# Kernel optimization log

Measured on AMD Instinct MI355X. Metric: run time of the kernel, lower is better.

Reference implementation:

```python
import jax, jax.numpy as jnp
import numpy as np

B, T, D, P, M = 4, 1024, 512, 64, 256


def setup_inputs() -> dict:
    key = jax.random.key(0)
    ks = jax.random.split(key, 10)
    s_d = 1.0 / np.sqrt(D)
    s_m = 1.0 / np.sqrt(M)
    s_p = 1.0 / np.sqrt(P)
    return {
        "inputs": jax.random.normal(ks[0], (B, T, D), dtype=jnp.float32),
        "ec": jax.random.normal(ks[1], (B, M), dtype=jnp.float32),
        "W1": jax.random.uniform(ks[2], (D, P), jnp.float32, -s_d, s_d),
        "b1": jax.random.uniform(ks[3], (P,), jnp.float32, -s_d, s_d),
        "W2": jax.random.uniform(ks[4], (D, P), jnp.float32, -s_d, s_d),
        "b2": jax.random.uniform(ks[5], (P,), jnp.float32, -s_d, s_d),
        "W3": jax.random.uniform(ks[6], (M, P), jnp.float32, -s_m, s_m),
        "b3": jax.random.uniform(ks[7], (P,), jnp.float32, -s_m, s_m),
        "wa_w": jax.random.uniform(ks[8], (P,), jnp.float32, -s_p, s_p),
        "wa_b": jax.random.uniform(ks[9], (), jnp.float32, -s_p, s_p),
    }


def reference(inputs, ec, W1, b1, W2, b2, W3, b3, wa_w, wa_b):
    # inputs: (B,T,D), ec: (B,M)
    w1h = inputs @ W1 + b1          # (B,T,P)
    w2h = inputs @ W2 + b2          # (B,T,P)
    w3e = ec @ W3 + b3              # (B,P)
    # Gt: (B,T,T,P) via broadcast add + tanh
    gt = jnp.tanh(w1h[:, :, None, :] + w2h[:, None, :, :] + w3e[:, None, None, :])
    at = jnp.einsum('btup,p->btu', gt, wa_w) + wa_b   # (B,T,T)
    at = jax.nn.softmax(at, axis=-1)
    out = jnp.einsum('btu,bud->btd', at, inputs)      # (B,T,D)
    return out
```

## Files before the change

### kernel.cpp

```cpp
#include <hip/hip_runtime.h>
#include <hip/hip_bf16.h>

constexpr int BB = 4;
constexpr int TT = 1024;
constexpr int DD = 512;
constexpr int PP = 64;
constexpr int MM = 256;

constexpr float CSCALE = 2.8853900817779268f;
constexpr float L2E = 1.4426950408889634f;

typedef __attribute__((ext_vector_type(8))) short v8s;
typedef __attribute__((ext_vector_type(4))) float v4f;
typedef unsigned int __attribute__((address_space(1))) gu32;
typedef unsigned int __attribute__((address_space(3))) su32;

__device__ __forceinline__ unsigned short f2bf(float f) {
    unsigned u = __builtin_bit_cast(unsigned, f);
    unsigned r = (u + 0x7fffu + ((u >> 16) & 1u)) >> 16;
    return (unsigned short)r;
}
__device__ __forceinline__ float bf2f(unsigned short h) {
    return __builtin_bit_cast(float, (unsigned)h << 16);
}
__device__ __forceinline__ void split2(float v, unsigned short& h, unsigned short& l) {
    unsigned short hh = f2bf(v);
    h = hh;
    l = f2bf(v - bf2f(hh));
}
__device__ __forceinline__ void gld_lds16(const void* g, void* l) {
    __builtin_amdgcn_global_load_lds((const gu32*)g, (su32*)l, 16, 0, 0);
}

__global__ __launch_bounds__(256) void prep1_kernel(
    const float* __restrict__ x, const float* __restrict__ ec,
    const float* __restrict__ W1, const float* __restrict__ W2,
    const float* __restrict__ W3, const float* __restrict__ b3,
    unsigned short* __restrict__ xt,
    unsigned short* __restrict__ WhT, unsigned short* __restrict__ WlT,
    float* __restrict__ E3) {
    __shared__ float tile[64][65];
    int bid = blockIdx.x;
    int tid = threadIdx.x;
    if (bid < 512) {
        int d0 = (bid & 7) << 6;
        int u0 = ((bid >> 3) & 15) << 6;
        int b = bid >> 7;
        int c4 = (tid & 15) << 2, r = tid >> 4;
        #pragma unroll
        for (int i = 0; i < 4; i++) {
            int row = r + (i << 4);
            float4 v = *(const float4*)(x + ((size_t)b * TT + u0 + row) * DD + d0 + c4);
            tile[row][c4 + 0] = v.x;
            tile[row][c4 + 1] = v.y;
            tile[row][c4 + 2] = v.z;
            tile[row][c4 + 3] = v.w;
        }
        __syncthreads();
        int dd = tid >> 2;
        int uq = (tid & 3) << 4;
        unsigned short us[16];
        #pragma unroll
        for (int j = 0; j < 16; j++) us[j] = f2bf(tile[uq + j][dd]);
        uint4 w0, w1;
        w0.x = us[0] | ((unsigned)us[1] << 16);  w0.y = us[2] | ((unsigned)us[3] << 16);
        w0.z = us[4] | ((unsigned)us[5] << 16);  w0.w = us[6] | ((unsigned)us[7] << 16);
        w1.x = us[8] | ((unsigned)us[9] << 16);  w1.y = us[10] | ((unsigned)us[11] << 16);
        w1.z = us[12] | ((unsigned)us[13] << 16); w1.w = us[14] | ((unsigned)us[15] << 16);
        unsigned short* dst = xt + ((size_t)b * DD + d0 + dd) * TT + u0 + uq;
        *(uint4*)dst = w0;
        *(uint4*)(dst + 8) = w1;
    } else if (bid < 528) {
        int w = bid - 512;
        int n = tid >> 1;
        int kb = (w << 5) + ((tid & 1) << 4);
        unsigned short hs[16], ls[16];
        #pragma unroll
        for (int kk = 0; kk < 16; kk++) {
            int k = kb + kk;
            float v = (n < 64) ? W1[k * PP + n] : W2[k * PP + (n - 64)];
            split2(v, hs[kk], ls[kk]);
        }
        uint4 a, bqq;
        a.x = hs[0] | ((unsigned)hs[1] << 16);   a.y = hs[2] | ((unsigned)hs[3] << 16);
        a.z = hs[4] | ((unsigned)hs[5] << 16);   a.w = hs[6] | ((unsigned)hs[7] << 16);
        bqq.x = hs[8] | ((unsigned)hs[9] << 16); bqq.y = hs[10] | ((unsigned)hs[11] << 16);
        bqq.z = hs[12] | ((unsigned)hs[13] << 16); bqq.w = hs[14] | ((unsigned)hs[15] << 16);
        *(uint4*)(WhT + (size_t)n * DD + kb) = a;
        *(uint4*)(WhT + (size_t)n * DD + kb + 8) = bqq;
        a.x = ls[0] | ((unsigned)ls[1] << 16);   a.y = ls[2] | ((unsigned)ls[3] << 16);
        a.z = ls[4] | ((unsigned)ls[5] << 16);   a.w = ls[6] | ((unsigned)ls[7] << 16);
        bqq.x = ls[8] | ((unsigned)ls[9] << 16); bqq.y = ls[10] | ((unsigned)ls[11] << 16);
        bqq.z = ls[12] | ((unsigned)ls[13] << 16); bqq.w = ls[14] | ((unsigned)ls[15] << 16);
        *(uint4*)(WlT + (size_t)n * DD + kb) = a;
        *(uint4*)(WlT + (size_t)n * DD + kb + 8) = bqq;
    } else {
        int b = tid >> 6, p = tid & 63;
        float a = b3[p];
        const float* e = ec + (size_t)b * MM;
        #pragma unroll 4
        for (int m = 0; m < MM; m++) a = fmaf(e[m], W3[m * PP + p], a);
        E3[b * PP + p] = __builtin_amdgcn_exp2f(a * CSCALE);
    }
}

__global__ __launch_bounds__(256) void prep2_kernel(
    const float* __restrict__ x,
    const unsigned short* __restrict__ WhT, const unsigned short* __restrict__ WlT,
    const float* __restrict__ b1, const float* __restrict__ b2,
    float* __restrict__ E1, float* __restrict__ E2) {
    __shared__ unsigned short AsH[16][72];
    __shared__ unsigned short AsL[16][72];
    __shared__ unsigned short BsH[128][72];
    __shared__ unsigned short BsL[128][72];
    int m0 = blockIdx.x << 4;
    int tid = threadIdx.x;
    int lane = tid & 63;
    int wv = tid >> 6;
    int wn = wv << 5;
    int l15 = lane & 15;
    int quad = lane >> 4;

    v4f acc[2];
    acc[0] = (v4f){0.f, 0.f, 0.f, 0.f};
    acc[1] = acc[0];

    for (int k0 = 0; k0 < DD; k0 += 64) {
        __syncthreads();
        {
            int row = tid >> 4, k4 = (tid & 15) << 2;
            float4 v = *(const float4*)(x + (size_t)(m0 + row) * DD + k0 + k4);
            unsigned short h0, h1, h2, h3, l0, l1, l2, l3;
            split2(v.x, h0, l0); split2(v.y, h1, l1);
            split2(v.z, h2, l2); split2(v.w, h3, l3);
            uint2 hw, lw;
            hw.x = h0 | ((unsigned)h1 << 16); hw.y = h2 | ((unsigned)h3 << 16);
            lw.x = l0 | ((unsigned)l1 << 16); lw.y = l2 | ((unsigned)l3 << 16);
            *(uint2*)&AsH[row][k4] = hw;
            *(uint2*)&AsL[row][k4] = lw;
        }
        #pragma unroll
        for (int i = 0; i < 4; i++) {
            int s = (i << 8) + tid;
            int row = s >> 3, k8 = (s & 7) << 3;
            *(uint4*)&BsH[row][k8] = *(const uint4*)(WhT + (size_t)row * DD + k0 + k8);
            *(uint4*)&BsL[row][k8] = *(const uint4*)(WlT + (size_t)row * DD + k0 + k8);
        }
        __syncthreads();
        #pragma unroll
        for (int kk = 0; kk < 64; kk += 32) {
            int kc = kk + (quad << 3);
            v8s aH0 = *(const v8s*)&AsH[l15][kc];
            v8s aL0 = *(const v8s*)&AsL[l15][kc];
            #pragma unroll
            for (int nt = 0; nt < 2; nt++) {
                v8s bH = *(const v8s*)&BsH[wn + (nt << 4) + l15][kc];
                v8s bL = *(const v8s*)&BsL[wn + (nt << 4) + l15][kc];
                acc[nt] = __builtin_amdgcn_mfma_f32_16x16x32_bf16(aH0, bH, acc[nt], 0, 0, 0);
                acc[nt] = __builtin_amdgcn_mfma_f32_16x16x32_bf16(aH0, bL, acc[nt], 0, 0, 0);
                acc[nt] = __builtin_amdgcn_mfma_f32_16x16x32_bf16(aL0, bH, acc[nt], 0, 0, 0);
            }
        }
    }
    #pragma unroll
    for (int nt = 0; nt < 2; nt++) {
        int n = wn + (nt << 4) + l15;
        int p = n & 63;
        float bias = (n < 64) ? b1[p] : b2[p];
        float* E = (n < 64) ? E1 : E2;
        int rbase = m0 + (quad << 2);
        #pragma unroll
        for (int r = 0; r < 4; r++) {
            float h = acc[nt][r] + bias;
            E[(size_t)(rbase + r) * PP + p] = __builtin_amdgcn_exp2f(h * CSCALE);
        }
    }
}

__global__ __launch_bounds__(256, 4) void scores_kernel(
    const float* __restrict__ E1, const float* __restrict__ E2,
    const float* __restrict__ E3, const float* __restrict__ wa_w,
    const float* __restrict__ wa_b, unsigned short* __restrict__ at_bf) {
    __shared__ float sm[4][4];
    __shared__ float sl[4][4];
    int tid = threadIdx.x;
    int bid = blockIdx.x;
    int b = bid >> 8;
    int t0 = (bid & 255) << 2;
    int pp = tid & 7;
    int uu = tid >> 3;
    int p0 = pp << 3;
    int lane = tid & 63;
    int wv = tid >> 6;
    int my_i = pp & 3;
    bool pbit1 = (pp & 2) != 0;
    bool pbit0 = (pp & 1) != 0;

    float ww2[8], H[4][8];
    float base;
    {
        float4 wv0 = *(const float4*)(wa_w + p0);
        float4 wv1 = *(const float4*)(wa_w + p0 + 4);
        float s = wv0.x + wv0.y + wv0.z + wv0.w + wv1.x + wv1.y + wv1.z + wv1.w;
        s += __shfl_xor(s, 1, 64);
        s += __shfl_xor(s, 2, 64);
        s += __shfl_xor(s, 4, 64);
        base = (s + wa_b[0]) * L2E;
        ww2[0] = -2.f * L2E * wv0.x; ww2[1] = -2.f * L2E * wv0.y;
        ww2[2] = -2.f * L2E * wv0.z; ww2[3] = -2.f * L2E * wv0.w;
        ww2[4] = -2.f * L2E * wv1.x; ww2[5] = -2.f * L2E * wv1.y;
        ww2[6] = -2.f * L2E * wv1.z; ww2[7] = -2.f * L2E * wv1.w;
        float4 e3a = *(const float4*)(E3 + (b << 6) + p0);
        float4 e3b = *(const float4*)(E3 + (b << 6) + p0 + 4);
        #pragma unroll
        for (int i = 0; i < 4; i++) {
            const float* e1p = E1 + (((size_t)(b << 10) + t0 + i) << 6) + p0;
            float4 a = *(const float4*)e1p;
            float4 c = *(const float4*)(e1p + 4);
            H[i][0] = a.x * e3a.x; H[i][1] = a.y * e3a.y; H[i][2] = a.z * e3a.z; H[i][3] = a.w * e3a.w;
            H[i][4] = c.x * e3b.x; H[i][5] = c.y * e3b.y; H[i][6] = c.z * e3b.z; H[i][7] = c.w * e3b.w;
        }
    }

    float own[32];
    float mown = -1e30f;
    #pragma unroll
    for (int k = 0; k < 32; k++) {
        int u = (k << 5) + uu;
        const float* ep = E2 + (((size_t)(b << 10) + u) << 6) + p0;
        float4 e0 = *(const float4*)ep;
        float4 e1 = *(const float4*)(ep + 4);
        float ev[8] = {e0.x, e0.y, e0.z, e0.w, e1.x, e1.y, e1.z, e1.w};
        float sr_[4];
        #pragma unroll
        for (int i = 0; i < 4; i++) {
            float d0 = fmaf(H[i][0], ev[0], 1.0f);
            float d1 = fmaf(H[i][1], ev[1], 1.0f);
            float d2 = fmaf(H[i][2], ev[2], 1.0f);
            float d3 = fmaf(H[i][3], ev[3], 1.0f);
            float d4 = fmaf(H[i][4], ev[4], 1.0f);
            float d5 = fmaf(H[i][5], ev[5], 1.0f);
            float d6 = fmaf(H[i][6], ev[6], 1.0f);
            float d7 = fmaf(H[i][7], ev[7], 1.0f);
            float e01 = d0 * d1, e23 = d2 * d3, e45 = d4 * d5, e67 = d6 * d7;
            float n01 = fmaf(ww2[0], d1, ww2[1] * d0);
            float n23 = fmaf(ww2[2], d3, ww2[3] * d2);
            float n45 = fmaf(ww2[4], d5, ww2[5] * d4);
            float n67 = fmaf(ww2[6], d7, ww2[7] * d6);
            float q03 = e01 * e23, q47 = e45 * e67;
            float n03 = fmaf(n23, e01, n01 * e23);
            float n47 = fmaf(n67, e45, n45 * e67);
            float Dq = q03 * q47;
            float Nq = fmaf(n47, q03, n03 * q47);
            sr_[i] = Nq * __builtin_amdgcn_rcpf(Dq);
        }
        float s0 = sr_[0], s1 = sr_[1], s2 = sr_[2], s3 = sr_[3];
        s0 += __shfl_xor(s0, 4, 64);
        s1 += __shfl_xor(s1, 4, 64);
        s2 += __shfl_xor(s2, 4, 64);
        s3 += __shfl_xor(s3, 4, 64);
        float op0 = pbit1 ? s2 : s0;
        float op1 = pbit1 ? s3 : s1;
        float ot0 = pbit1 ? s0 : s2;
        float ot1 = pbit1 ? s1 : s3;
        op0 += __shfl_xor(ot0, 2, 64);
        op1 += __shfl_xor(ot1, 2, 64);
        float osel = pbit0 ? op1 : op0;
        float osnd = pbit0 ? op0 : op1;
        osel += __shfl_xor(osnd, 1, 64);
        float o = osel + base;
        own[k] = o;
        mown = fmaxf(mown, o);
    }
    mown = fmaxf(mown, __shfl_xor(mown, 8, 64));
    mown = fmaxf(mown, __shfl_xor(mown, 16, 64));
    mown = fmaxf(mown, __shfl_xor(mown, 32, 64));
    if (lane < 4) sm[wv][lane] = mown;
    __syncthreads();
    float mx = fmaxf(fmaxf(sm[0][my_i], sm[1][my_i]), fmaxf(sm[2][my_i], sm[3][my_i]));

    float l = 0.f;
    #pragma unroll
    for (int k = 0; k < 32; k++) {
        float e = __builtin_amdgcn_exp2f(own[k] - mx);
        own[k] = e;
        l += e;
    }
    l += __shfl_xor(l, 8, 64);
    l += __shfl_xor(l, 16, 64);
    l += __shfl_xor(l, 32, 64);
    if (lane < 4) sl[wv][lane] = l;
    __syncthreads();
    float inv = 1.0f / (sl[0][my_i] + sl[1][my_i] + sl[2][my_i] + sl[3][my_i]);

    if (pp < 4) {
        size_t rowbase = ((size_t)((b << 10) + t0 + my_i)) << 10;
        #pragma unroll
        for (int k = 0; k < 32; k++) {
            at_bf[rowbase + (k << 5) + uu] = f2bf(own[k] * inv);
        }
    }
}

__global__ __launch_bounds__(256) void av_mfma_kernel(
    const unsigned short* __restrict__ at_bf, const unsigned short* __restrict__ xt,
    float* __restrict__ out) {
    __shared__ unsigned short As[64 * 64];
    __shared__ unsigned short Bs[64 * 64];
    int b = blockIdx.z;
    int m0 = blockIdx.y << 6;
    int n0 = blockIdx.x << 6;
    const unsigned short* A = at_bf + ((size_t)b << 20);
    const unsigned short* Bt = xt + (size_t)b * DD * TT;
    int tid = threadIdx.x;
    int lane = tid & 63;
    int wv = tid >> 6;
    int wm = (wv & 1) << 5;
    int wn = (wv >> 1) << 5;
    int l15 = lane & 15;
    int quad = lane >> 4;

    int sr = lane >> 3;
    int scg = (lane & 7) ^ sr;

    v4f acc00 = {0.f, 0.f, 0.f, 0.f}, acc01 = acc00, acc10 = acc00, acc11 = acc00;

    for (int k0 = 0; k0 < TT; k0 += 64) {
        __syncthreads();
        #pragma unroll
        for (int t = 0; t < 2; t++) {
            int r0 = (wv << 4) + (t << 3);
            int row = r0 + sr;
            gld_lds16(A + (size_t)(m0 + row) * TT + k0 + (scg << 3), &As[r0 << 6]);
            gld_lds16(Bt + (size_t)(n0 + row) * TT + k0 + (scg << 3), &Bs[r0 << 6]);
        }
        __syncthreads();
        #pragma unroll
        for (int kq = 0; kq < 2; kq++) {
            int c = (kq << 2) + quad;
            int swz = (c ^ (l15 & 7)) << 3;
            v8s a0 = *(const v8s*)&As[((wm + l15) << 6) + swz];
            v8s a1 = *(const v8s*)&As[((wm + 16 + l15) << 6) + swz];
            v8s b0 = *(const v8s*)&Bs[((wn + l15) << 6) + swz];
            v8s b1 = *(const v8s*)&Bs[((wn + 16 + l15) << 6) + swz];
            acc00 = __builtin_amdgcn_mfma_f32_16x16x32_bf16(a0, b0, acc00, 0, 0, 0);
            acc01 = __builtin_amdgcn_mfma_f32_16x16x32_bf16(a0, b1, acc01, 0, 0, 0);
            acc10 = __builtin_amdgcn_mfma_f32_16x16x32_bf16(a1, b0, acc10, 0, 0, 0);
            acc11 = __builtin_amdgcn_mfma_f32_16x16x32_bf16(a1, b1, acc11, 0, 0, 0);
        }
    }
    float* C = out + (size_t)b * TT * DD;
    int rbase = m0 + wm + (quad << 2);
    int cn = n0 + wn + l15;
    #pragma unroll
    for (int r = 0; r < 4; r++) {
        C[(size_t)(rbase + r) * DD + cn]           = acc00[r];
        C[(size_t)(rbase + r) * DD + cn + 16]      = acc01[r];
        C[(size_t)(rbase + 16 + r) * DD + cn]      = acc10[r];
        C[(size_t)(rbase + 16 + r) * DD + cn + 16] = acc11[r];
    }
}

extern "C" void kernel_launch(void* const* d_in, const int* in_sizes, int n_in,
                              void* d_out, int out_size, void* d_ws, size_t ws_size,
                              hipStream_t stream) {
    const float* inputs = (const float*)d_in[0];
    const float* ec     = (const float*)d_in[1];
    const float* W1     = (const float*)d_in[2];
    const float* b1     = (const float*)d_in[3];
    const float* W2     = (const float*)d_in[4];
    const float* b2     = (const float*)d_in[5];
    const float* W3     = (const float*)d_in[6];
    const float* b3     = (const float*)d_in[7];
    const float* wa_w   = (const float*)d_in[8];
    const float* wa_b   = (const float*)d_in[9];
    float* out = (float*)d_out;

    float* ws = (float*)d_ws;
    float* E1 = ws;
    float* E2 = ws + 262144;
    float* E3 = ws + 524288;
    unsigned short* at_bf = (unsigned short*)(ws + 524800);
    unsigned short* xt    = (unsigned short*)(ws + 524800 + 2097152);
    unsigned short* WhT   = at_bf;
    unsigned short* WlT   = at_bf + 65536;

    hipLaunchKernelGGL(prep1_kernel, dim3(529), dim3(256), 0, stream,
                       inputs, ec, W1, W2, W3, b3, xt, WhT, WlT, E3);
    hipLaunchKernelGGL(prep2_kernel, dim3(256), dim3(256), 0, stream,
                       inputs, WhT, WlT, b1, b2, E1, E2);
    hipLaunchKernelGGL(scores_kernel, dim3(1024), dim3(256), 0, stream,
                       E1, E2, E3, wa_w, wa_b, at_bf);
    hipLaunchKernelGGL(av_mfma_kernel, dim3(DD / 64, TT / 64, BB), dim3(256), 0, stream,
                       at_bf, xt, out);
}
```

Measured before the change: 146.7 us.

## Double-buffer LDS tiles in prep2 and AV GEMM, split prep2 N across grid

Both the projection GEMM (prep2) and the attention-times-values GEMM now use two LDS buffers, so the next k-tile loads while MFMAs run on the current one, with one barrier per iteration instead of two. prep2 also gains a second grid dimension that splits the 128 output columns (W1 vs W2 halves) across blocks, doubling the block count and halving per-block work. The cost is twice the LDS per block, which may lower occupancy, and prep2 now converts the x tile to hi/lo bf16 in both halves, doubling that work.

```diff
diff --git a/kernel.cpp b/kernel.cpp
--- a/kernel.cpp
+++ b/kernel.cpp
@@ -109,24 +109,24 @@
     const unsigned short* __restrict__ WhT, const unsigned short* __restrict__ WlT,
     const float* __restrict__ b1, const float* __restrict__ b2,
     float* __restrict__ E1, float* __restrict__ E2) {
-    __shared__ unsigned short AsH[16][72];
-    __shared__ unsigned short AsL[16][72];
-    __shared__ unsigned short BsH[128][72];
-    __shared__ unsigned short BsL[128][72];
+    __shared__ unsigned short AsH[2][16][72];
+    __shared__ unsigned short AsL[2][16][72];
+    __shared__ unsigned short BsH[2][64][72];
+    __shared__ unsigned short BsL[2][64][72];
     int m0 = blockIdx.x << 4;
+    int half = blockIdx.y;
+    const unsigned short* WhTh = WhT + (size_t)(half << 6) * DD;
+    const unsigned short* WlTh = WlT + (size_t)(half << 6) * DD;
     int tid = threadIdx.x;
     int lane = tid & 63;
     int wv = tid >> 6;
-    int wn = wv << 5;
+    int wn = wv << 4;
     int l15 = lane & 15;
     int quad = lane >> 4;
 
-    v4f acc[2];
-    acc[0] = (v4f){0.f, 0.f, 0.f, 0.f};
-    acc[1] = acc[0];
-
-    for (int k0 = 0; k0 < DD; k0 += 64) {
-        __syncthreads();
+    v4f acc = (v4f){0.f, 0.f, 0.f, 0.f};
+
+    auto stage = [&](int buf, int k0) {
         {
             int row = tid >> 4, k4 = (tid & 15) << 2;
             float4 v = *(const float4*)(x + (size_t)(m0 + row) * DD + k0 + k4);
@@ -136,42 +136,44 @@
             uint2 hw, lw;
             hw.x = h0 | ((unsigned)h1 << 16); hw.y = h2 | ((unsigned)h3 << 16);
             lw.x = l0 | ((unsigned)l1 << 16); lw.y = l2 | ((unsigned)l3 << 16);
-            *(uint2*)&AsH[row][k4] = hw;
-            *(uint2*)&AsL[row][k4] = lw;
-        }
-        #pragma unroll
-        for (int i = 0; i < 4; i++) {
+            *(uint2*)&AsH[buf][row][k4] = hw;
+            *(uint2*)&AsL[buf][row][k4] = lw;
+        }
+        #pragma unroll
+        for (int i = 0; i < 2; i++) {
             int s = (i << 8) + tid;
             int row = s >> 3, k8 = (s & 7) << 3;
-            *(uint4*)&BsH[row][k8] = *(const uint4*)(WhT + (size_t)row * DD + k0 + k8);
-            *(uint4*)&BsL[row][k8] = *(const uint4*)(WlT + (size_t)row * DD + k0 + k8);
-        }
-        __syncthreads();
+            *(uint4*)&BsH[buf][row][k8] = *(const uint4*)(WhTh + (size_t)row * DD + k0 + k8);
+            *(uint4*)&BsL[buf][row][k8] = *(const uint4*)(WlTh + (size_t)row * DD + k0 + k8);
+        }
+    };
+
+    stage(0, 0);
+    __syncthreads();
+    for (int it = 0; it < 8; it++) {
+        int cur = it & 1;
+        if (it < 7) stage(cur ^ 1, (it + 1) << 6);
         #pragma unroll
         for (int kk = 0; kk < 64; kk += 32) {
             int kc = kk + (quad << 3);
-            v8s aH0 = *(const v8s*)&AsH[l15][kc];
-            v8s aL0 = *(const v8s*)&AsL[l15][kc];
-            #pragma unroll
-            for (int nt = 0; nt < 2; nt++) {
-                v8s bH = *(const v8s*)&BsH[wn + (nt << 4) + l15][kc];
-                v8s bL = *(const v8s*)&BsL[wn + (nt << 4) + l15][kc];
-                acc[nt] = __builtin_amdgcn_mfma_f32_16x16x32_bf16(aH0, bH, acc[nt], 0, 0, 0);
-                acc[nt] = __builtin_amdgcn_mfma_f32_16x16x32_bf16(aH0, bL, acc[nt], 0, 0, 0);
-                acc[nt] = __builtin_amdgcn_mfma_f32_16x16x32_bf16(aL0, bH, acc[nt], 0, 0, 0);
-            }
-        }
-    }
-    #pragma unroll
-    for (int nt = 0; nt < 2; nt++) {
-        int n = wn + (nt << 4) + l15;
-        int p = n & 63;
-        float bias = (n < 64) ? b1[p] : b2[p];
-        float* E = (n < 64) ? E1 : E2;
+            v8s aH0 = *(const v8s*)&AsH[cur][l15][kc];
+            v8s aL0 = *(const v8s*)&AsL[cur][l15][kc];
+            v8s bH = *(const v8s*)&BsH[cur][wn + l15][kc];
+            v8s bL = *(const v8s*)&BsL[cur][wn + l15][kc];
+            acc = __builtin_amdgcn_mfma_f32_16x16x32_bf16(aH0, bH, acc, 0, 0, 0);
+            acc = __builtin_amdgcn_mfma_f32_16x16x32_bf16(aH0, bL, acc, 0, 0, 0);
+            acc = __builtin_amdgcn_mfma_f32_16x16x32_bf16(aL0, bH, acc, 0, 0, 0);
+        }
+        __syncthreads();
+    }
+    {
+        int p = wn + l15;
+        float bias = half ? b2[p] : b1[p];
+        float* E = half ? E2 : E1;
         int rbase = m0 + (quad << 2);
         #pragma unroll
         for (int r = 0; r < 4; r++) {
-            float h = acc[nt][r] + bias;
+            float h = acc[r] + bias;
             E[(size_t)(rbase + r) * PP + p] = __builtin_amdgcn_exp2f(h * CSCALE);
         }
     }
@@ -305,8 +307,8 @@
 __global__ __launch_bounds__(256) void av_mfma_kernel(
     const unsigned short* __restrict__ at_bf, const unsigned short* __restrict__ xt,
     float* __restrict__ out) {
-    __shared__ unsigned short As[64 * 64];
-    __shared__ unsigned short Bs[64 * 64];
+    __shared__ unsigned short As[2][64 * 64];
+    __shared__ unsigned short Bs[2][64 * 64];
     int b = blockIdx.z;
     int m0 = blockIdx.y << 6;
     int n0 = blockIdx.x << 6;
@@ -325,29 +327,35 @@
 
     v4f acc00 = {0.f, 0.f, 0.f, 0.f}, acc01 = acc00, acc10 = acc00, acc11 = acc00;
 
-    for (int k0 = 0; k0 < TT; k0 += 64) {
-        __syncthreads();
+    auto stage = [&](int buf, int k0) {
         #pragma unroll
         for (int t = 0; t < 2; t++) {
             int r0 = (wv << 4) + (t << 3);
             int row = r0 + sr;
-            gld_lds16(A + (size_t)(m0 + row) * TT + k0 + (scg << 3), &As[r0 << 6]);
-            gld_lds16(Bt + (size_t)(n0 + row) * TT + k0 + (scg << 3), &Bs[r0 << 6]);
-        }
-        __syncthreads();
+            gld_lds16(A + (size_t)(m0 + row) * TT + k0 + (scg << 3), &As[buf][r0 << 6]);
+            gld_lds16(Bt + (size_t)(n0 + row) * TT + k0 + (scg << 3), &Bs[buf][r0 << 6]);
+        }
+    };
+
+    stage(0, 0);
+    __syncthreads();
+    for (int it = 0; it < 16; it++) {
+        int cur = it & 1;
+        if (it < 15) stage(cur ^ 1, (it + 1) << 6);
         #pragma unroll
         for (int kq = 0; kq < 2; kq++) {
             int c = (kq << 2) + quad;
             int swz = (c ^ (l15 & 7)) << 3;
-            v8s a0 = *(const v8s*)&As[((wm + l15) << 6) + swz];
-            v8s a1 = *(const v8s*)&As[((wm + 16 + l15) << 6) + swz];
-            v8s b0 = *(const v8s*)&Bs[((wn + l15) << 6) + swz];
-            v8s b1 = *(const v8s*)&Bs[((wn + 16 + l15) << 6) + swz];
+            v8s a0 = *(const v8s*)&As[cur][((wm + l15) << 6) + swz];
+            v8s a1 = *(const v8s*)&As[cur][((wm + 16 + l15) << 6) + swz];
+            v8s b0 = *(const v8s*)&Bs[cur][((wn + l15) << 6) + swz];
+            v8s b1 = *(const v8s*)&Bs[cur][((wn + 16 + l15) << 6) + swz];
             acc00 = __builtin_amdgcn_mfma_f32_16x16x32_bf16(a0, b0, acc00, 0, 0, 0);
             acc01 = __builtin_amdgcn_mfma_f32_16x16x32_bf16(a0, b1, acc01, 0, 0, 0);
             acc10 = __builtin_amdgcn_mfma_f32_16x16x32_bf16(a1, b0, acc10, 0, 0, 0);
             acc11 = __builtin_amdgcn_mfma_f32_16x16x32_bf16(a1, b1, acc11, 0, 0, 0);
         }
+        __syncthreads();
     }
     float* C = out + (size_t)b * TT * DD;
     int rbase = m0 + wm + (quad << 2);
@@ -387,7 +395,7 @@
 
     hipLaunchKernelGGL(prep1_kernel, dim3(529), dim3(256), 0, stream,
                        inputs, ec, W1, W2, W3, b3, xt, WhT, WlT, E3);
-    hipLaunchKernelGGL(prep2_kernel, dim3(256), dim3(256), 0, stream,
+    hipLaunchKernelGGL(prep2_kernel, dim3(256, 2), dim3(256), 0, stream,
                        inputs, WhT, WlT, b1, b2, E1, E2);
     hipLaunchKernelGGL(scores_kernel, dim3(1024), dim3(256), 0, stream,
                        E1, E2, E3, wa_w, wa_b, at_bf);
```

Measured after the change: 150.1 us. 1.02x slower.
